# Kernel optimization log

Measured on AMD Instinct MI355X. Metric: run time of the kernel, lower is better.

## Reference

```python
import jax, jax.numpy as jnp
import numpy as np
from jax import lax

# norse LIFParameters defaults: tau_syn_inv=200, tau_mem_inv=100, v_leak=0,
# v_th=1, v_reset=0, dt=0.001; alpha=0.5 (super-spike surrogate slope).
DT = 1e-3
TAU_SYN_INV = 200.0
TAU_MEM_INV = 100.0
V_LEAK = 0.0
V_TH = 1.0
V_RESET = 0.0
ALPHA = 0.5
NUM_STEPS = 100


@jax.custom_vjp
def heaviside_super(x):
    # forward: hard threshold; backward: SuperSpike surrogate (norse.threshold)
    return (x > 0).astype(x.dtype)

def _hs_fwd(x):
    return heaviside_super(x), x

def _hs_bwd(x, g):
    return (g / (ALPHA * jnp.abs(x) + 1.0) ** 2,)

heaviside_super.defvjp(_hs_fwd, _hs_bwd)


def lif_step(cur, v, i):
    # norse lif_step: Euler update of membrane v and synaptic current i
    v_dec = v + DT * TAU_MEM_INV * ((V_LEAK - v) + i)
    i_dec = i * (1.0 - DT * TAU_SYN_INV)
    z = heaviside_super(v_dec - V_TH)
    v_new = (1.0 - z) * v_dec + z * V_RESET
    i_new = i_dec + cur
    return z, v_new, i_new


def conv2d(x, w, b):
    y = lax.conv_general_dilated(x, w, window_strides=(1, 1), padding='VALID',
                                 dimension_numbers=('NCHW', 'OIHW', 'NCHW'))
    return y + b[None, :, None, None]


def maxpool2(x):
    return lax.reduce_window(x, -jnp.inf, lax.max, (1, 1, 2, 2), (1, 1, 2, 2), 'VALID')


def snn_forward(x, w1, b1, w2, b2, wf, bf):
    B = x.shape[0]
    # conv1(x) is identical every timestep in the torch code; hoist it.
    cur1 = maxpool2(conv2d(x, w1, b1))  # [B,13,6,6]
    v1 = jnp.zeros_like(cur1); i1 = jnp.zeros_like(cur1)
    v2 = jnp.zeros((B, w2.shape[0], 3, 3), x.dtype); i2 = jnp.zeros_like(v2)
    v3 = jnp.zeros((B, wf.shape[0]), x.dtype); i3 = jnp.zeros_like(v3)

    def step(carry, _):
        v1, i1, v2, i2, v3, i3 = carry
        spk1, v1, i1 = lif_step(cur1, v1, i1)          # [B,13,6,6]
        cur2 = conv2d(spk1, w2, b2)                    # [B,64,3,3]
        spk2, v2, i2 = lif_step(cur2, v2, i2)
        cur3 = spk2.reshape(B, -1) @ wf.T + bf         # [B,2]
        spk3, v3, i3 = lif_step(cur3, v3, i3)
        return (v1, i1, v2, i2, v3, i3), (spk3, v3)

    _, (spk3_seq, v3_seq) = lax.scan(step, (v1, i1, v2, i2, v3, i3), None, length=NUM_STEPS)
    spk_out = spk3_seq.sum(0)   # sum of output spikes over time, [B,2]
    return spk_out, v3_seq      # v3_seq = stacked mem3_record, [T,B,2]


def setup_inputs() -> dict:
    key = jax.random.key(0)
    ks = jax.random.split(key, 7)
    B = 2048
    x = jax.random.normal(ks[0], (B, 1, 16, 16), jnp.float32)
    w1 = jax.random.normal(ks[1], (13, 1, 4, 4), jnp.float32) * 0.25
    b1 = jax.random.normal(ks[2], (13,), jnp.float32) * 0.1
    w2 = jax.random.normal(ks[3], (64, 13, 4, 4), jnp.float32) * (1.0 / np.sqrt(13 * 16))
    b2 = jax.random.normal(ks[4], (64,), jnp.float32) * 0.05
    wf = jax.random.normal(ks[5], (2, 576), jnp.float32) * (1.0 / np.sqrt(576))
    bf = jax.random.normal(ks[6], (2,), jnp.float32) * 0.05
    return {"x": x, "w1": w1, "b1": b1, "w2": w2, "b2": b2, "wf": wf, "bf": bf}


def reference(x, w1, b1, w2, b2, wf, bf):
    return snn_forward(x, w1, b1, w2, b2, wf, bf)
```

## Files before the change

### kernel.cpp

```cpp
#include <hip/hip_runtime.h>


#define NSTEPS 100
#define IMSTRIDE 272
#define ZIMG (48 * IMSTRIDE)
#define Z2W 612
#define Z2P (4 * Z2W)

typedef __attribute__((ext_vector_type(4))) int i32x4;

__device__ __forceinline__ void conv1_row(const float* __restrict__ xs,
                                          const float* __restrict__ w1s,
                                          float b1v, int y, float* cur) {
    float cr[2][12];
    #pragma unroll
    for (int rr = 0; rr < 2; ++rr) {
        const int cy = 2 * y + rr;
        #pragma unroll
        for (int cx = 0; cx < 12; ++cx) {
            float a = 0.f;
            #pragma unroll
            for (int ky = 0; ky < 4; ++ky)
            #pragma unroll
            for (int kx = 0; kx < 4; ++kx)
                a = fmaf(xs[(cy + ky) * 16 + cx + kx], w1s[ky * 4 + kx], a);
            cr[rr][cx] = a + b1v;
        }
    }
    #pragma unroll
    for (int px = 0; px < 6; ++px)
        cur[px] = fmaxf(fmaxf(cr[0][2 * px], cr[0][2 * px + 1]),
                        fmaxf(cr[1][2 * px], cr[1][2 * px + 1]));
}

__device__ __forceinline__ void lif1_row(float* v1, float* i1, const float* cur,
                                         unsigned char* pb, int ic, int y) {
    unsigned zb[6];
    #pragma unroll
    for (int xx = 0; xx < 6; ++xx) {
        const float vd = v1[xx] + 0.1f * (i1[xx] - v1[xx]);
        i1[xx] = i1[xx] * 0.8f + cur[xx];
        const bool sp = vd > 1.0f;
        v1[xx] = sp ? 0.0f : vd;
        zb[xx] = sp ? 1u : 0u;
    }
    const unsigned q0 = zb[0] | (zb[1] << 8) | (zb[2] << 16) | (zb[3] << 24);
    const unsigned q1 = zb[1] | (zb[2] << 8) | (zb[3] << 16) | (zb[4] << 24);
    const unsigned q2 = zb[2] | (zb[3] << 8) | (zb[4] << 16) | (zb[5] << 24);
    #pragma unroll
    for (int ky = 0; ky < 4; ++ky) {
        const int py = y - ky;
        if (0 <= py && py <= 2) {
            unsigned char* b = pb - ky * (3 * IMSTRIDE) + 4 * ((ky + ic) & 3);
            *(unsigned*)(b)                = q0;
            *(unsigned*)(b + IMSTRIDE)     = q1;
            *(unsigned*)(b + 2 * IMSTRIDE) = q2;
        }
    }
}

__global__ __launch_bounds__(256, 2)
void snn_kernel(const float* __restrict__ x,
                const float* __restrict__ w1,
                const float* __restrict__ b1,
                const float* __restrict__ w2,
                const float* __restrict__ b2,
                const float* __restrict__ wf,
                const float* __restrict__ bf,
                float* __restrict__ out, int B)
{
    __shared__ __align__(16) unsigned char s_im[2 * ZIMG];
    __shared__ __align__(16) float s_z2[2 * Z2P];
    __shared__ __align__(16) float s_w1[13 * 16];
    __shared__ float s_b1[13];

    const int tid  = threadIdx.x;
    const int wave = tid >> 6, lane = tid & 63;
    const int quad = lane >> 4, col = lane & 15;

    ((float4*)(s_z2 + wave * Z2W))[lane] =
        ((const float4*)(x + (size_t)(blockIdx.x * 4 + wave) * 256))[lane];
    if (tid < 208) s_w1[tid] = w1[tid];
    if (tid < 13)  s_b1[tid] = b1[tid];
    for (int i = tid; i < 2 * ZIMG / 16; i += 256)
        ((uint4*)s_im)[i] = make_uint4(0, 0, 0, 0);
    __syncthreads();

    int sA, icA, yA, sB = 0, icB = 0, yB = 0;
    { const int R = tid;       sA = R / 78; int r = R - 78 * sA; icA = r / 6; yA = r - 6 * icA; }
    if (tid < 56) { const int R = tid + 256; sB = R / 78; int r = R - 78 * sB; icB = r / 6; yB = r - 6 * icB; }

    float cur1a[6], v1a[6], i1a[6], cur1b[6], v1b[6], i1b[6];
    conv1_row(s_z2 + sA * Z2W, s_w1 + icA * 16, s_b1[icA], yA, cur1a);
    if (tid < 56) conv1_row(s_z2 + sB * Z2W, s_w1 + icB * 16, s_b1[icB], yB, cur1b);
    #pragma unroll
    for (int j = 0; j < 6; ++j) { v1a[j] = i1a[j] = 0.f; v1b[j] = i1b[j] = 0.f; }

    const int pbOffA = (9 * sA + 3 * yA) * IMSTRIDE + 16 * icA;
    const int pbOffB = (9 * sB + 3 * yB) * IMSTRIDE + 16 * icB;

    i32x4 A1[4], A2[4], A3[4];
    float Mrow;
    {
        const float* wrow = w2 + (size_t)(wave * 16 + col) * 208;
        float M = 1e-20f;
        for (int k = 0; k < 208; ++k) M = fmaxf(M, fabsf(wrow[k]));
        Mrow = M;
        const float inv = 127.0f / M;
        const float q1s = M * (1.0f / 127.0f);
        const float q2s = M * (1.0f / (127.0f * 127.0f));
        #pragma unroll
        for (int kt = 0; kt < 4; ++kt) {
            i32x4 w1v = {0, 0, 0, 0}, w2v = {0, 0, 0, 0}, w3v = {0, 0, 0, 0};
            #pragma unroll
            for (int j = 0; j < 16; ++j) {
                const int kp = kt * 64 + quad * 16 + j;
                const int W = kp >> 2, kx = kp & 3;
                const int ic = W >> 2, ky = ((W & 3) - ic) & 3;
                const float w = (ic < 13) ? wrow[ic * 16 + ky * 4 + kx] : 0.f;
                const float b1f = rintf(w * inv);
                const float r1  = fmaf(b1f, -q1s, w);
                const float b2f = rintf(r1 * inv * 127.0f);
                const float r2  = fmaf(b2f, -q2s, r1);
                const float b3f = rintf(r2 * inv * 127.0f * 127.0f);
                const int wi = j >> 2, sh = (j & 3) * 8;
                w1v[wi] |= ((int)b1f & 0xFF) << sh;
                w2v[wi] |= ((int)b2f & 0xFF) << sh;
                w3v[wi] |= ((int)b3f & 0xFF) << sh;
            }
            A1[kt] = w1v; A2[kt] = w2v; A3[kt] = w3v;
        }
    }
    float sc1[4], sc2[4], sc3[4];
    #pragma unroll
    for (int r = 0; r < 4; ++r) {
        const float Mr = __shfl(Mrow, quad * 4 + r);
        sc1[r] = Mr * (1.0f / 127.0f);
        sc2[r] = Mr * (1.0f / (127.0f * 127.0f));
        sc3[r] = Mr * (1.0f / (127.0f * 127.0f * 127.0f));
    }

    float wf0[9], wf1[9];
    #pragma unroll
    for (int q = 0; q < 9; ++q) {
        wf0[q] = wf[lane * 9 + q];
        wf1[q] = wf[576 + lane * 9 + q];
    }
    const float bfv0 = bf[0], bfv1 = bf[1];
    float b2r[4];
    #pragma unroll
    for (int r = 0; r < 4; ++r) b2r[r] = b2[wave * 16 + quad * 4 + r];

    const unsigned char* bp[3];
    int zoff[3];
    bool zv[3];
    #pragma unroll
    for (int nt = 0; nt < 3; ++nt) {
        const int n = nt * 16 + col;
        bp[nt] = s_im + n * IMSTRIDE + quad * 16;
        zv[nt] = (n < 36);
        const int slz = n / 9, pos = n - slz * 9;
        zoff[nt] = slz * Z2W + pos * 68 + wave * 16 + quad * 4;
    }

    float v2[12], i2[12];
    #pragma unroll
    for (int p = 0; p < 12; ++p) { v2[p] = 0.f; i2[p] = 0.f; }
    float v3a = 0.f, i3a = 0.f, v3b = 0.f, i3b = 0.f, sum0 = 0.f, sum1 = 0.f;

    const int sG = blockIdx.x * 4 + wave;
    float* outv = out + (size_t)2 * B;

    auto do_fc = [&](int tp) {
        const float* zs = s_z2 + (tp & 1) * Z2P + wave * Z2W;
        float p0 = 0.f, p1 = 0.f;
        #pragma unroll
        for (int q = 0; q < 9; ++q) {
            const float z = zs[q * 68 + lane];
            p0 = fmaf(z, wf0[q], p0);
            p1 = fmaf(z, wf1[q], p1);
        }
        #pragma unroll
        for (int off = 32; off > 0; off >>= 1) {
            p0 += __shfl_xor(p0, off);
            p1 += __shfl_xor(p1, off);
        }
        const float c3a = p0 + bfv0, c3b = p1 + bfv1;
        const float vd0 = v3a + 0.1f * (i3a - v3a);
        const float vd1 = v3b + 0.1f * (i3b - v3b);
        i3a = i3a * 0.8f + c3a;
        i3b = i3b * 0.8f + c3b;
        const bool q0 = vd0 > 1.0f, q1 = vd1 > 1.0f;
        v3a = q0 ? 0.0f : vd0;
        v3b = q1 ? 0.0f : vd1;
        sum0 += q0 ? 1.0f : 0.0f;
        sum1 += q1 ? 1.0f : 0.0f;
        if (lane == 0)
            *(float2*)(outv + (size_t)tp * 2 * B + 2 * sG) = make_float2(v3a, v3b);
    };

    auto step = [&](int t, int P) {
        unsigned char* zb = s_im + P * ZIMG;
        lif1_row(v1a, i1a, cur1a, zb + pbOffA, icA, yA);
        if (tid < 56) lif1_row(v1b, i1b, cur1b, zb + pbOffB, icB, yB);
        __syncthreads();

        if (t) do_fc(t - 1);

        i32x4 c1a = {0,0,0,0}, c1b = c1a, c1c = c1a;
        i32x4 c2a = c1a, c2b = c1a, c2c = c1a;
        i32x4 c3a_ = c1a, c3b_ = c1a, c3c = c1a;
        const int zo = P * ZIMG;
        #pragma unroll
        for (int kt = 0; kt < 4; ++kt) {
            const i32x4 B0 = *(const i32x4*)(bp[0] + zo + kt * 64);
            const i32x4 B1 = *(const i32x4*)(bp[1] + zo + kt * 64);
            const i32x4 B2 = *(const i32x4*)(bp[2] + zo + kt * 64);
            c1a = __builtin_amdgcn_mfma_i32_16x16x64_i8(A1[kt], B0, c1a, 0, 0, 0);
            c1b = __builtin_amdgcn_mfma_i32_16x16x64_i8(A1[kt], B1, c1b, 0, 0, 0);
            c1c = __builtin_amdgcn_mfma_i32_16x16x64_i8(A1[kt], B2, c1c, 0, 0, 0);
            c2a = __builtin_amdgcn_mfma_i32_16x16x64_i8(A2[kt], B0, c2a, 0, 0, 0);
            c2b = __builtin_amdgcn_mfma_i32_16x16x64_i8(A2[kt], B1, c2b, 0, 0, 0);
            c2c = __builtin_amdgcn_mfma_i32_16x16x64_i8(A2[kt], B2, c2c, 0, 0, 0);
            c3a_ = __builtin_amdgcn_mfma_i32_16x16x64_i8(A3[kt], B0, c3a_, 0, 0, 0);
            c3b_ = __builtin_amdgcn_mfma_i32_16x16x64_i8(A3[kt], B1, c3b_, 0, 0, 0);
            c3c = __builtin_amdgcn_mfma_i32_16x16x64_i8(A3[kt], B2, c3c, 0, 0, 0);
        }

        const i32x4 L1[3] = {c1a, c1b, c1c};
        const i32x4 L2[3] = {c2a, c2b, c2c};
        const i32x4 L3[3] = {c3a_, c3b_, c3c};
        float* z2p = s_z2 + P * Z2P;
        #pragma unroll
        for (int nt = 0; nt < 3; ++nt) {
            float4 zq;
            float* zqf = (float*)&zq;
            #pragma unroll
            for (int r = 0; r < 4; ++r) {
                const int p = nt * 4 + r;
                const float cur2 =
                    fmaf(sc1[r], (float)L1[nt][r],
                    fmaf(sc2[r], (float)L2[nt][r],
                    fmaf(sc3[r], (float)L3[nt][r], b2r[r])));
                const float vd = v2[p] + 0.1f * (i2[p] - v2[p]);
                i2[p] = i2[p] * 0.8f + cur2;
                const bool sp = vd > 1.0f;
                v2[p] = sp ? 0.0f : vd;
                zqf[r] = sp ? 1.0f : 0.0f;
            }
            if (zv[nt]) *(float4*)(z2p + zoff[nt]) = zq;
        }
    };

    __syncthreads();

    #pragma unroll 1
    for (int t = 0; t < NSTEPS; t += 2) {
        step(t, 0);
        step(t + 1, 1);
    }

    __syncthreads();
    do_fc(NSTEPS - 1);

    if (lane == 0)
        *(float2*)(out + (size_t)2 * sG) = make_float2(sum0, sum1);
}

extern "C" void kernel_launch(void* const* d_in, const int* in_sizes, int n_in,
                              void* d_out, int out_size, void* d_ws, size_t ws_size,
                              hipStream_t stream)
{
    const float* x  = (const float*)d_in[0];
    const float* w1 = (const float*)d_in[1];
    const float* b1 = (const float*)d_in[2];
    const float* w2 = (const float*)d_in[3];
    const float* b2 = (const float*)d_in[4];
    const float* wf = (const float*)d_in[5];
    const float* bf = (const float*)d_in[6];
    float* out = (float*)d_out;

    const int B = in_sizes[0] / 256;
    const int grid = B / 4;

    hipLaunchKernelGGL(snn_kernel, dim3(grid), dim3(256), 0, stream,
                       x, w1, b1, w2, b2, wf, bf, out, B);
}
```

Before: 271.3 us.

## Batch two timesteps per barrier and store layer-2 spikes as bf16

```diff
diff --git a/kernel.cpp b/kernel.cpp
--- a/kernel.cpp
+++ b/kernel.cpp
@@ -2,10 +2,12 @@
 
 
 #define NSTEPS 100
+#define NCHUNK 50
 #define IMSTRIDE 272
 #define ZIMG (48 * IMSTRIDE)
-#define Z2W 612
-#define Z2P (4 * Z2W)
+#define Z2S 612
+#define Z2T (4 * Z2S)
+#define Z2PAR (2 * Z2T)
 
 typedef __attribute__((ext_vector_type(4))) int i32x4;
 
@@ -69,8 +71,9 @@
                 const float* __restrict__ bf,
                 float* __restrict__ out, int B)
 {
-    __shared__ __align__(16) unsigned char s_im[2 * ZIMG];
-    __shared__ __align__(16) float s_z2[2 * Z2P];
+    __shared__ __align__(16) unsigned char s_im[4 * ZIMG];
+    __shared__ __align__(16) unsigned short s_z2h[2 * Z2PAR];
+    __shared__ __align__(16) float s_x[4 * 256];
     __shared__ __align__(16) float s_w1[13 * 16];
     __shared__ float s_b1[13];
 
@@ -78,11 +81,11 @@
     const int wave = tid >> 6, lane = tid & 63;
     const int quad = lane >> 4, col = lane & 15;
 
-    ((float4*)(s_z2 + wave * Z2W))[lane] =
+    ((float4*)(s_x + wave * 256))[lane] =
         ((const float4*)(x + (size_t)(blockIdx.x * 4 + wave) * 256))[lane];
     if (tid < 208) s_w1[tid] = w1[tid];
     if (tid < 13)  s_b1[tid] = b1[tid];
-    for (int i = tid; i < 2 * ZIMG / 16; i += 256)
+    for (int i = tid; i < 4 * ZIMG / 16; i += 256)
         ((uint4*)s_im)[i] = make_uint4(0, 0, 0, 0);
     __syncthreads();
 
@@ -91,8 +94,8 @@
     if (tid < 56) { const int R = tid + 256; sB = R / 78; int r = R - 78 * sB; icB = r / 6; yB = r - 6 * icB; }
 
     float cur1a[6], v1a[6], i1a[6], cur1b[6], v1b[6], i1b[6];
-    conv1_row(s_z2 + sA * Z2W, s_w1 + icA * 16, s_b1[icA], yA, cur1a);
-    if (tid < 56) conv1_row(s_z2 + sB * Z2W, s_w1 + icB * 16, s_b1[icB], yB, cur1b);
+    conv1_row(s_x + sA * 256, s_w1 + icA * 16, s_b1[icA], yA, cur1a);
+    if (tid < 56) conv1_row(s_x + sB * 256, s_w1 + icB * 16, s_b1[icB], yB, cur1b);
     #pragma unroll
     for (int j = 0; j < 6; ++j) { v1a[j] = i1a[j] = 0.f; v1b[j] = i1b[j] = 0.f; }
 
@@ -151,16 +154,16 @@
     #pragma unroll
     for (int r = 0; r < 4; ++r) b2r[r] = b2[wave * 16 + quad * 4 + r];
 
-    const unsigned char* bp[3];
-    int zoff[3];
+    int bpo[3];
+    int zwo[3];
     bool zv[3];
     #pragma unroll
     for (int nt = 0; nt < 3; ++nt) {
         const int n = nt * 16 + col;
-        bp[nt] = s_im + n * IMSTRIDE + quad * 16;
+        bpo[nt] = n * IMSTRIDE + quad * 16;
         zv[nt] = (n < 36);
         const int slz = n / 9, pos = n - slz * 9;
-        zoff[nt] = slz * Z2W + pos * 68 + wave * 16 + quad * 4;
+        zwo[nt] = slz * Z2S + pos * 68 + wave * 16 + quad * 4;
     }
 
     float v2[12], i2[12];
@@ -171,12 +174,11 @@
     const int sG = blockIdx.x * 4 + wave;
     float* outv = out + (size_t)2 * B;
 
-    auto do_fc = [&](int tp) {
-        const float* zs = s_z2 + (tp & 1) * Z2P + wave * Z2W;
+    auto fc_step = [&](const unsigned short* zs, int tp) {
         float p0 = 0.f, p1 = 0.f;
         #pragma unroll
         for (int q = 0; q < 9; ++q) {
-            const float z = zs[q * 68 + lane];
+            const float z = __uint_as_float(((unsigned)zs[q * 68 + lane]) << 16);
             p0 = fmaf(z, wf0[q], p0);
             p1 = fmaf(z, wf1[q], p1);
         }
@@ -199,69 +201,84 @@
             *(float2*)(outv + (size_t)tp * 2 * B + 2 * sG) = make_float2(v3a, v3b);
     };
 
-    auto step = [&](int t, int P) {
-        unsigned char* zb = s_im + P * ZIMG;
-        lif1_row(v1a, i1a, cur1a, zb + pbOffA, icA, yA);
-        if (tid < 56) lif1_row(v1b, i1b, cur1b, zb + pbOffB, icB, yB);
+    auto chunk = [&](int ch, int P) {
+        unsigned char* zb0 = s_im + (2 * P) * ZIMG;
+        unsigned char* zb1 = s_im + (2 * P + 1) * ZIMG;
+        lif1_row(v1a, i1a, cur1a, zb0 + pbOffA, icA, yA);
+        if (tid < 56) lif1_row(v1b, i1b, cur1b, zb0 + pbOffB, icB, yB);
+        lif1_row(v1a, i1a, cur1a, zb1 + pbOffA, icA, yA);
+        if (tid < 56) lif1_row(v1b, i1b, cur1b, zb1 + pbOffB, icB, yB);
         __syncthreads();
 
-        if (t) do_fc(t - 1);
-
-        i32x4 c1a = {0,0,0,0}, c1b = c1a, c1c = c1a;
-        i32x4 c2a = c1a, c2b = c1a, c2c = c1a;
-        i32x4 c3a_ = c1a, c3b_ = c1a, c3c = c1a;
-        const int zo = P * ZIMG;
-        #pragma unroll
-        for (int kt = 0; kt < 4; ++kt) {
-            const i32x4 B0 = *(const i32x4*)(bp[0] + zo + kt * 64);
-            const i32x4 B1 = *(const i32x4*)(bp[1] + zo + kt * 64);
-            const i32x4 B2 = *(const i32x4*)(bp[2] + zo + kt * 64);
-            c1a = __builtin_amdgcn_mfma_i32_16x16x64_i8(A1[kt], B0, c1a, 0, 0, 0);
-            c1b = __builtin_amdgcn_mfma_i32_16x16x64_i8(A1[kt], B1, c1b, 0, 0, 0);
-            c1c = __builtin_amdgcn_mfma_i32_16x16x64_i8(A1[kt], B2, c1c, 0, 0, 0);
-            c2a = __builtin_amdgcn_mfma_i32_16x16x64_i8(A2[kt], B0, c2a, 0, 0, 0);
-            c2b = __builtin_amdgcn_mfma_i32_16x16x64_i8(A2[kt], B1, c2b, 0, 0, 0);
-            c2c = __builtin_amdgcn_mfma_i32_16x16x64_i8(A2[kt], B2, c2c, 0, 0, 0);
-            c3a_ = __builtin_amdgcn_mfma_i32_16x16x64_i8(A3[kt], B0, c3a_, 0, 0, 0);
-            c3b_ = __builtin_amdgcn_mfma_i32_16x16x64_i8(A3[kt], B1, c3b_, 0, 0, 0);
-            c3c = __builtin_amdgcn_mfma_i32_16x16x64_i8(A3[kt], B2, c3c, 0, 0, 0);
-        }
-
-        const i32x4 L1[3] = {c1a, c1b, c1c};
-        const i32x4 L2[3] = {c2a, c2b, c2c};
-        const i32x4 L3[3] = {c3a_, c3b_, c3c};
-        float* z2p = s_z2 + P * Z2P;
-        #pragma unroll
-        for (int nt = 0; nt < 3; ++nt) {
-            float4 zq;
-            float* zqf = (float*)&zq;
-            #pragma unroll
-            for (int r = 0; r < 4; ++r) {
-                const int p = nt * 4 + r;
-                const float cur2 =
-                    fmaf(sc1[r], (float)L1[nt][r],
-                    fmaf(sc2[r], (float)L2[nt][r],
-                    fmaf(sc3[r], (float)L3[nt][r], b2r[r])));
-                const float vd = v2[p] + 0.1f * (i2[p] - v2[p]);
-                i2[p] = i2[p] * 0.8f + cur2;
-                const bool sp = vd > 1.0f;
-                v2[p] = sp ? 0.0f : vd;
-                zqf[r] = sp ? 1.0f : 0.0f;
+        if (ch) {
+            const unsigned short* zp = s_z2h + (P ^ 1) * Z2PAR + wave * Z2S;
+            fc_step(zp, 2 * ch - 2);
+            fc_step(zp + Z2T, 2 * ch - 1);
+        }
+
+        #pragma unroll
+        for (int tl = 0; tl < 2; ++tl) {
+            const unsigned char* zbuf = s_im + (2 * P + tl) * ZIMG;
+            i32x4 c1a = {0,0,0,0}, c1b = c1a, c1c = c1a;
+            i32x4 c2a = c1a, c2b = c1a, c2c = c1a;
+            i32x4 c3a_ = c1a, c3b_ = c1a, c3c = c1a;
+            #pragma unroll
+            for (int kt = 0; kt < 4; ++kt) {
+                const i32x4 B0 = *(const i32x4*)(zbuf + bpo[0] + kt * 64);
+                const i32x4 B1 = *(const i32x4*)(zbuf + bpo[1] + kt * 64);
+                const i32x4 B2v = *(const i32x4*)(zbuf + bpo[2] + kt * 64);
+                c1a = __builtin_amdgcn_mfma_i32_16x16x64_i8(A1[kt], B0,  c1a, 0, 0, 0);
+                c1b = __builtin_amdgcn_mfma_i32_16x16x64_i8(A1[kt], B1,  c1b, 0, 0, 0);
+                c1c = __builtin_amdgcn_mfma_i32_16x16x64_i8(A1[kt], B2v, c1c, 0, 0, 0);
+                c2a = __builtin_amdgcn_mfma_i32_16x16x64_i8(A2[kt], B0,  c2a, 0, 0, 0);
+                c2b = __builtin_amdgcn_mfma_i32_16x16x64_i8(A2[kt], B1,  c2b, 0, 0, 0);
+                c2c = __builtin_amdgcn_mfma_i32_16x16x64_i8(A2[kt], B2v, c2c, 0, 0, 0);
+                c3a_ = __builtin_amdgcn_mfma_i32_16x16x64_i8(A3[kt], B0,  c3a_, 0, 0, 0);
+                c3b_ = __builtin_amdgcn_mfma_i32_16x16x64_i8(A3[kt], B1,  c3b_, 0, 0, 0);
+                c3c = __builtin_amdgcn_mfma_i32_16x16x64_i8(A3[kt], B2v, c3c, 0, 0, 0);
             }
-            if (zv[nt]) *(float4*)(z2p + zoff[nt]) = zq;
+
+            const i32x4 L1[3] = {c1a, c1b, c1c};
+            const i32x4 L2[3] = {c2a, c2b, c2c};
+            const i32x4 L3[3] = {c3a_, c3b_, c3c};
+            unsigned short* z2b = s_z2h + P * Z2PAR + tl * Z2T;
+            #pragma unroll
+            for (int nt = 0; nt < 3; ++nt) {
+                unsigned zbits[4];
+                #pragma unroll
+                for (int r = 0; r < 4; ++r) {
+                    const int p = nt * 4 + r;
+                    const float cur2 =
+                        fmaf(sc1[r], (float)L1[nt][r],
+                        fmaf(sc2[r], (float)L2[nt][r],
+                        fmaf(sc3[r], (float)L3[nt][r], b2r[r])));
+                    const float vd = v2[p] + 0.1f * (i2[p] - v2[p]);
+                    i2[p] = i2[p] * 0.8f + cur2;
+                    const bool sp = vd > 1.0f;
+                    v2[p] = sp ? 0.0f : vd;
+                    zbits[r] = sp ? 0x3F80u : 0u;
+                }
+                if (zv[nt]) {
+                    const unsigned lo = zbits[0] | (zbits[1] << 16);
+                    const unsigned hi = zbits[2] | (zbits[3] << 16);
+                    *(uint2*)(z2b + zwo[nt]) = make_uint2(lo, hi);
+                }
+            }
         }
     };
 
+    #pragma unroll 1
+    for (int cc = 0; cc < NCHUNK; cc += 2) {
+        chunk(cc, 0);
+        chunk(cc + 1, 1);
+    }
+
     __syncthreads();
-
-    #pragma unroll 1
-    for (int t = 0; t < NSTEPS; t += 2) {
-        step(t, 0);
-        step(t + 1, 1);
-    }
-
-    __syncthreads();
-    do_fc(NSTEPS - 1);
+    {
+        const unsigned short* zp = s_z2h + 1 * Z2PAR + wave * Z2S;
+        fc_step(zp, NSTEPS - 2);
+        fc_step(zp + Z2T, NSTEPS - 1);
+    }
 
     if (lane == 0)
         *(float2*)(out + (size_t)2 * sG) = make_float2(sum0, sum1);
```

New measurement: 270.5 us. No clear change (-0.3%).

## Halve samples per block, store layer-2 spikes as bf16, raise occupancy

Applied to the files above, without the earlier changes.

```diff
diff --git a/kernel.cpp b/kernel.cpp
--- a/kernel.cpp
+++ b/kernel.cpp
@@ -3,9 +3,10 @@
 
 #define NSTEPS 100
 #define IMSTRIDE 272
-#define ZIMG (48 * IMSTRIDE)
-#define Z2W 612
-#define Z2P (4 * Z2W)
+#define NCOLS 32
+#define ZIMG (NCOLS * IMSTRIDE)
+#define Z2S 612
+#define Z2PAR (2 * Z2S)
 
 typedef __attribute__((ext_vector_type(4))) int i32x4;
 
@@ -59,7 +60,7 @@
     }
 }
 
-__global__ __launch_bounds__(256, 2)
+__global__ __launch_bounds__(256, 4)
 void snn_kernel(const float* __restrict__ x,
                 const float* __restrict__ w1,
                 const float* __restrict__ b1,
@@ -70,7 +71,8 @@
                 float* __restrict__ out, int B)
 {
     __shared__ __align__(16) unsigned char s_im[2 * ZIMG];
-    __shared__ __align__(16) float s_z2[2 * Z2P];
+    __shared__ __align__(16) unsigned short s_z2h[2 * Z2PAR];
+    __shared__ __align__(16) float s_x[2 * 256];
     __shared__ __align__(16) float s_w1[13 * 16];
     __shared__ float s_b1[13];
 
@@ -78,26 +80,24 @@
     const int wave = tid >> 6, lane = tid & 63;
     const int quad = lane >> 4, col = lane & 15;
 
-    ((float4*)(s_z2 + wave * Z2W))[lane] =
-        ((const float4*)(x + (size_t)(blockIdx.x * 4 + wave) * 256))[lane];
+    if (tid < 128)
+        ((float4*)s_x)[tid] = ((const float4*)(x + (size_t)blockIdx.x * 512))[tid];
     if (tid < 208) s_w1[tid] = w1[tid];
     if (tid < 13)  s_b1[tid] = b1[tid];
     for (int i = tid; i < 2 * ZIMG / 16; i += 256)
         ((uint4*)s_im)[i] = make_uint4(0, 0, 0, 0);
     __syncthreads();
 
-    int sA, icA, yA, sB = 0, icB = 0, yB = 0;
-    { const int R = tid;       sA = R / 78; int r = R - 78 * sA; icA = r / 6; yA = r - 6 * icA; }
-    if (tid < 56) { const int R = tid + 256; sB = R / 78; int r = R - 78 * sB; icB = r / 6; yB = r - 6 * icB; }
-
-    float cur1a[6], v1a[6], i1a[6], cur1b[6], v1b[6], i1b[6];
-    conv1_row(s_z2 + sA * Z2W, s_w1 + icA * 16, s_b1[icA], yA, cur1a);
-    if (tid < 56) conv1_row(s_z2 + sB * Z2W, s_w1 + icB * 16, s_b1[icB], yB, cur1b);
-    #pragma unroll
-    for (int j = 0; j < 6; ++j) { v1a[j] = i1a[j] = 0.f; v1b[j] = i1b[j] = 0.f; }
-
-    const int pbOffA = (9 * sA + 3 * yA) * IMSTRIDE + 16 * icA;
-    const int pbOffB = (9 * sB + 3 * yB) * IMSTRIDE + 16 * icB;
+    const bool rowOwner = (tid < 156);
+    int sA = 0, icA = 0, yA = 0;
+    if (rowOwner) { sA = tid / 78; const int r = tid - 78 * sA; icA = r / 6; yA = r - 6 * icA; }
+
+    float cur1a[6], v1a[6], i1a[6];
+    if (rowOwner) conv1_row(s_x + sA * 256, s_w1 + icA * 16, s_b1[icA], yA, cur1a);
+    #pragma unroll
+    for (int j = 0; j < 6; ++j) { v1a[j] = 0.f; i1a[j] = 0.f; }
+
+    const int pbOff = (9 * sA + 3 * yA) * IMSTRIDE + 16 * icA;
 
     i32x4 A1[4], A2[4], A3[4];
     float Mrow;
@@ -151,32 +151,31 @@
     #pragma unroll
     for (int r = 0; r < 4; ++r) b2r[r] = b2[wave * 16 + quad * 4 + r];
 
-    const unsigned char* bp[3];
-    int zoff[3];
-    bool zv[3];
-    #pragma unroll
-    for (int nt = 0; nt < 3; ++nt) {
+    int bpo[2];
+    int zwo[2];
+    bool zv[2];
+    #pragma unroll
+    for (int nt = 0; nt < 2; ++nt) {
         const int n = nt * 16 + col;
-        bp[nt] = s_im + n * IMSTRIDE + quad * 16;
-        zv[nt] = (n < 36);
+        bpo[nt] = n * IMSTRIDE + quad * 16;
+        zv[nt] = (n < 18);
         const int slz = n / 9, pos = n - slz * 9;
-        zoff[nt] = slz * Z2W + pos * 68 + wave * 16 + quad * 4;
-    }
-
-    float v2[12], i2[12];
-    #pragma unroll
-    for (int p = 0; p < 12; ++p) { v2[p] = 0.f; i2[p] = 0.f; }
+        zwo[nt] = slz * Z2S + pos * 68 + wave * 16 + quad * 4;
+    }
+
+    float v2[8], i2[8];
+    #pragma unroll
+    for (int p = 0; p < 8; ++p) { v2[p] = 0.f; i2[p] = 0.f; }
     float v3a = 0.f, i3a = 0.f, v3b = 0.f, i3b = 0.f, sum0 = 0.f, sum1 = 0.f;
 
-    const int sG = blockIdx.x * 4 + wave;
+    const int sG = blockIdx.x * 2 + wave;
     float* outv = out + (size_t)2 * B;
 
-    auto do_fc = [&](int tp) {
-        const float* zs = s_z2 + (tp & 1) * Z2P + wave * Z2W;
+    auto fc_step = [&](const unsigned short* zs, int tp) {
         float p0 = 0.f, p1 = 0.f;
         #pragma unroll
         for (int q = 0; q < 9; ++q) {
-            const float z = zs[q * 68 + lane];
+            const float z = __uint_as_float(((unsigned)zs[q * 68 + lane]) << 16);
             p0 = fmaf(z, wf0[q], p0);
             p1 = fmaf(z, wf1[q], p1);
         }
@@ -200,41 +199,35 @@
     };
 
     auto step = [&](int t, int P) {
-        unsigned char* zb = s_im + P * ZIMG;
-        lif1_row(v1a, i1a, cur1a, zb + pbOffA, icA, yA);
-        if (tid < 56) lif1_row(v1b, i1b, cur1b, zb + pbOffB, icB, yB);
+        if (rowOwner) lif1_row(v1a, i1a, cur1a, s_im + P * ZIMG + pbOff, icA, yA);
         __syncthreads();
 
-        if (t) do_fc(t - 1);
-
-        i32x4 c1a = {0,0,0,0}, c1b = c1a, c1c = c1a;
-        i32x4 c2a = c1a, c2b = c1a, c2c = c1a;
-        i32x4 c3a_ = c1a, c3b_ = c1a, c3c = c1a;
-        const int zo = P * ZIMG;
+        if (t && wave < 2)
+            fc_step(s_z2h + (P ^ 1) * Z2PAR + wave * Z2S, t - 1);
+
+        const unsigned char* zbuf = s_im + P * ZIMG;
+        i32x4 c1a = {0,0,0,0}, c1b = c1a;
+        i32x4 c2a = c1a, c2b = c1a;
+        i32x4 c3a_ = c1a, c3b_ = c1a;
         #pragma unroll
         for (int kt = 0; kt < 4; ++kt) {
-            const i32x4 B0 = *(const i32x4*)(bp[0] + zo + kt * 64);
-            const i32x4 B1 = *(const i32x4*)(bp[1] + zo + kt * 64);
-            const i32x4 B2 = *(const i32x4*)(bp[2] + zo + kt * 64);
-            c1a = __builtin_amdgcn_mfma_i32_16x16x64_i8(A1[kt], B0, c1a, 0, 0, 0);
-            c1b = __builtin_amdgcn_mfma_i32_16x16x64_i8(A1[kt], B1, c1b, 0, 0, 0);
-            c1c = __builtin_amdgcn_mfma_i32_16x16x64_i8(A1[kt], B2, c1c, 0, 0, 0);
-            c2a = __builtin_amdgcn_mfma_i32_16x16x64_i8(A2[kt], B0, c2a, 0, 0, 0);
-            c2b = __builtin_amdgcn_mfma_i32_16x16x64_i8(A2[kt], B1, c2b, 0, 0, 0);
-            c2c = __builtin_amdgcn_mfma_i32_16x16x64_i8(A2[kt], B2, c2c, 0, 0, 0);
+            const i32x4 B0 = *(const i32x4*)(zbuf + bpo[0] + kt * 64);
+            const i32x4 B1 = *(const i32x4*)(zbuf + bpo[1] + kt * 64);
+            c1a  = __builtin_amdgcn_mfma_i32_16x16x64_i8(A1[kt], B0, c1a, 0, 0, 0);
+            c1b  = __builtin_amdgcn_mfma_i32_16x16x64_i8(A1[kt], B1, c1b, 0, 0, 0);
+            c2a  = __builtin_amdgcn_mfma_i32_16x16x64_i8(A2[kt], B0, c2a, 0, 0, 0);
+            c2b  = __builtin_amdgcn_mfma_i32_16x16x64_i8(A2[kt], B1, c2b, 0, 0, 0);
             c3a_ = __builtin_amdgcn_mfma_i32_16x16x64_i8(A3[kt], B0, c3a_, 0, 0, 0);
             c3b_ = __builtin_amdgcn_mfma_i32_16x16x64_i8(A3[kt], B1, c3b_, 0, 0, 0);
-            c3c = __builtin_amdgcn_mfma_i32_16x16x64_i8(A3[kt], B2, c3c, 0, 0, 0);
-        }
-
-        const i32x4 L1[3] = {c1a, c1b, c1c};
-        const i32x4 L2[3] = {c2a, c2b, c2c};
-        const i32x4 L3[3] = {c3a_, c3b_, c3c};
-        float* z2p = s_z2 + P * Z2P;
-        #pragma unroll
-        for (int nt = 0; nt < 3; ++nt) {
-            float4 zq;
-            float* zqf = (float*)&zq;
+        }
+
+        const i32x4 L1[2] = {c1a, c1b};
+        const i32x4 L2[2] = {c2a, c2b};
+        const i32x4 L3[2] = {c3a_, c3b_};
+        unsigned short* z2b = s_z2h + P * Z2PAR;
+        #pragma unroll
+        for (int nt = 0; nt < 2; ++nt) {
+            unsigned zbits[4];
             #pragma unroll
             for (int r = 0; r < 4; ++r) {
                 const int p = nt * 4 + r;
@@ -246,13 +239,15 @@
                 i2[p] = i2[p] * 0.8f + cur2;
                 const bool sp = vd > 1.0f;
                 v2[p] = sp ? 0.0f : vd;
-                zqf[r] = sp ? 1.0f : 0.0f;
+                zbits[r] = sp ? 0x3F80u : 0u;
             }
-            if (zv[nt]) *(float4*)(z2p + zoff[nt]) = zq;
+            if (zv[nt]) {
+                const unsigned lo = zbits[0] | (zbits[1] << 16);
+                const unsigned hi = zbits[2] | (zbits[3] << 16);
+                *(uint2*)(z2b + zwo[nt]) = make_uint2(lo, hi);
+            }
         }
     };
-
-    __syncthreads();
 
     #pragma unroll 1
     for (int t = 0; t < NSTEPS; t += 2) {
@@ -261,9 +256,10 @@
     }
 
     __syncthreads();
-    do_fc(NSTEPS - 1);
-
-    if (lane == 0)
+    if (wave < 2)
+        fc_step(s_z2h + 1 * Z2PAR + wave * Z2S, NSTEPS - 1);
+
+    if (wave < 2 && lane == 0)
         *(float2*)(out + (size_t)2 * sG) = make_float2(sum0, sum1);
 }
 
@@ -281,7 +277,7 @@
     float* out = (float*)d_out;
 
     const int B = in_sizes[0] / 256;
-    const int grid = B / 4;
+    const int grid = B / 2;
 
     hipLaunchKernelGGL(snn_kernel, dim3(grid), dim3(256), 0, stream,
                        x, w1, b1, w2, b2, wf, bf, out, B);
```

New measurement: 955.2 us. 252% more time.
